# Kernel tuning notes

Hardware: AMD Instinct MI355X
Metric: run time of the kernel (lower is better)

## Reference

```python
import jax, jax.numpy as jnp
import numpy as np

D_MODEL = 1024
EXPERT_SIZE = 512
N_EXPERTS = 8
GROUP_SIZE = 32
BATCH = 32
SEQ = 2048
TEMPERATURE = 1.0


def setup_inputs() -> dict:
    key = jax.random.key(0)
    k_x, k_l1, k_l2, k_c = jax.random.split(key, 4)
    x = jax.random.normal(k_x, (BATCH, SEQ, D_MODEL), dtype=jnp.float32)
    # truncated-normal-style init approximated with normal scaled by 1/sqrt(fan_in)
    lin1 = jax.random.normal(k_l1, (N_EXPERTS, D_MODEL, EXPERT_SIZE), dtype=jnp.float32) * (D_MODEL ** -0.5)
    lin2 = jax.random.normal(k_l2, (N_EXPERTS, EXPERT_SIZE, D_MODEL), dtype=jnp.float32) * (EXPERT_SIZE ** -0.5)
    controller = jax.random.normal(k_c, (D_MODEL, N_EXPERTS), dtype=jnp.float32) * (D_MODEL ** -0.5)
    return {"x": x, "lin1": lin1, "lin2": lin2, "controller": controller}


def reference(x, lin1, lin2, controller):
    B, S, D = x.shape
    # group_tokens: sparsity_dim=0 -> transpose to (S, B, D), split batch into groups
    xg = jnp.transpose(x, (1, 0, 2)).reshape(S, B // GROUP_SIZE, GROUP_SIZE, D)  # (s, g, k, d)
    # controller logits, softmax over the group (token) axis k (dim=-2)
    logits = jnp.einsum("sgkd,de->sgke", xg, controller) / TEMPERATURE
    merge_w = jax.nn.softmax(logits, axis=-2)  # (s, g, k, e)
    emit_w = merge_w  # default: emit softmax over tokens, same temp -> reuse
    # merge: weighted sum of tokens per expert
    merged = jnp.einsum("sgke,sgkd->sged", merge_w, xg)  # (s, g, e, d)
    # per-expert MLP
    h = jax.nn.relu(jnp.einsum("sged,edf->sgef", merged, lin1))  # (s, g, e, f)
    expert_out = jnp.einsum("sgef,efd->sged", h, lin2)  # (s, g, e, d)
    # emit back to tokens
    out = jnp.einsum("sgke,sged->sgkd", emit_w, expert_out)  # (s, g, k, d)
    # redistribute: (S, B, D) -> (B, S, D)
    return jnp.transpose(out.reshape(S, B, D), (1, 0, 2))
```

## Files before the change

### kernel.cpp

```cpp
#include <hip/hip_runtime.h>
#include <hip/hip_bf16.h>

#define SS 2048
#define BB 32
#define DD 1024
#define FF 512
#define EE 8

typedef __attribute__((ext_vector_type(8))) short short8;
typedef __attribute__((ext_vector_type(8))) unsigned short ushort8v;
typedef __attribute__((ext_vector_type(4))) unsigned short ushort4v;
typedef __attribute__((ext_vector_type(4))) float f32x4;

__device__ inline unsigned short f2bf(float f) {
  union { float f; unsigned u; } v; v.f = f;
  return (unsigned short)((v.u + 0x7FFFu + ((v.u >> 16) & 1u)) >> 16);
}
__device__ inline float bf2f(unsigned short h) {
  union { unsigned u; float f; } v; v.u = ((unsigned)h) << 16;
  return v.f;
}

__global__ __launch_bounds__(256) void ctrl_transpose(
    const float* __restrict__ ctrl, float* __restrict__ ctrlT) {
  int i = blockIdx.x * 256 + threadIdx.x;
  int e = i >> 10, d = i & 1023;
  ctrlT[i] = ctrl[(size_t)d * EE + e];
}

__global__ __launch_bounds__(256) void transpose_bf16(
    const float* __restrict__ in, unsigned short* __restrict__ out, int K, int N) {
  __shared__ float tile[32][33];
  int e = blockIdx.z;
  const float* inp = in + (size_t)e * K * N;
  unsigned short* outp = out + (size_t)e * K * N;
  int k0 = blockIdx.x * 32, n0 = blockIdx.y * 32;
  int tx = threadIdx.x;
  int ty = threadIdx.y;
#pragma unroll
  for (int i = 0; i < 4; i++) {
    int k = ty + i * 8;
    tile[k][tx] = inp[(size_t)(k0 + k) * N + n0 + tx];
  }
  __syncthreads();
#pragma unroll
  for (int i = 0; i < 4; i++) {
    int n = ty + i * 8;
    outp[(size_t)(n0 + n) * K + k0 + tx] = f2bf(tile[tx][n]);
  }
}

__global__ __launch_bounds__(512) void ctrl_logits(
    const float* __restrict__ x,
    const float* __restrict__ ctrlT,
    float* __restrict__ lg) {
  int s = blockIdx.x;
  int t = threadIdx.x, lane = t & 63, w = t >> 6;
  __shared__ __align__(16) float cs[EE * DD];
  for (int i = t; i < EE * DD / 4; i += 512)
    *(float4*)&cs[i * 4] = *(const float4*)&ctrlT[i * 4];
  __syncthreads();

  float acc[4][8] = {};
#pragma unroll
  for (int i = 0; i < 4; i++) {
    int dbase = lane * 4 + i * 256;
    float4 c4[8];
#pragma unroll
    for (int e = 0; e < 8; e++) c4[e] = *(const float4*)&cs[e * DD + dbase];
#pragma unroll
    for (int j = 0; j < 4; j++) {
      int k = w * 4 + j;
      float4 xv = *(const float4*)&x[((size_t)k * SS + s) * DD + dbase];
#pragma unroll
      for (int e = 0; e < 8; e++)
        acc[j][e] += xv.x * c4[e].x + xv.y * c4[e].y + xv.z * c4[e].z + xv.w * c4[e].w;
    }
  }
#pragma unroll
  for (int off = 1; off < 64; off <<= 1)
#pragma unroll
    for (int j = 0; j < 4; j++)
#pragma unroll
      for (int e = 0; e < 8; e++)
        acc[j][e] += __shfl_xor(acc[j][e], off, 64);
  if (lane == 0) {
#pragma unroll
    for (int j = 0; j < 4; j++) {
      int k = w * 4 + j;
      float4 lo = {acc[j][0], acc[j][1], acc[j][2], acc[j][3]};
      float4 hi = {acc[j][4], acc[j][5], acc[j][6], acc[j][7]};
      float* p = &lg[((size_t)s * BB + k) * EE];
      *(float4*)p = lo;
      *(float4*)(p + 4) = hi;
    }
  }
}

__global__ __launch_bounds__(256) void softmax_merge(
    const float* __restrict__ x,
    const float* __restrict__ lg,
    unsigned short* __restrict__ merged,
    float* __restrict__ mw) {
  int s = blockIdx.x;
  int t = threadIdx.x;
  __shared__ __align__(16) float wl[BB][EE];
  wl[t >> 3][t & 7] = lg[(size_t)s * BB * EE + t];
  __syncthreads();
  if (t < 32) {
    float lgv[8], mx[8], p[8], sm[8];
#pragma unroll
    for (int e = 0; e < 8; e++) { lgv[e] = wl[t][e]; mx[e] = lgv[e]; }
#pragma unroll
    for (int off = 1; off < 32; off <<= 1)
#pragma unroll
      for (int e = 0; e < 8; e++)
        mx[e] = fmaxf(mx[e], __shfl_xor(mx[e], off, 64));
#pragma unroll
    for (int e = 0; e < 8; e++) { p[e] = __expf(lgv[e] - mx[e]); sm[e] = p[e]; }
#pragma unroll
    for (int off = 1; off < 32; off <<= 1)
#pragma unroll
      for (int e = 0; e < 8; e++)
        sm[e] += __shfl_xor(sm[e], off, 64);
    float wv[8];
#pragma unroll
    for (int e = 0; e < 8; e++) { wv[e] = p[e] / sm[e]; wl[t][e] = wv[e]; }
    float4 mv0 = {wv[0], wv[1], wv[2], wv[3]};
    float4 mv1 = {wv[4], wv[5], wv[6], wv[7]};
    float* mwp = &mw[((size_t)s * BB + t) * EE];
    *(float4*)mwp = mv0;
    *(float4*)(mwp + 4) = mv1;
  }
  __syncthreads();

  int d0 = t * 4;
  float a[8][4] = {};
#pragma unroll 4
  for (int k = 0; k < 32; k++) {
    float4 xv = *(const float4*)&x[((size_t)k * SS + s) * DD + d0];
    float4 wA = *(const float4*)&wl[k][0];
    float4 wB = *(const float4*)&wl[k][4];
    a[0][0] += wA.x * xv.x; a[0][1] += wA.x * xv.y; a[0][2] += wA.x * xv.z; a[0][3] += wA.x * xv.w;
    a[1][0] += wA.y * xv.x; a[1][1] += wA.y * xv.y; a[1][2] += wA.y * xv.z; a[1][3] += wA.y * xv.w;
    a[2][0] += wA.z * xv.x; a[2][1] += wA.z * xv.y; a[2][2] += wA.z * xv.z; a[2][3] += wA.z * xv.w;
    a[3][0] += wA.w * xv.x; a[3][1] += wA.w * xv.y; a[3][2] += wA.w * xv.z; a[3][3] += wA.w * xv.w;
    a[4][0] += wB.x * xv.x; a[4][1] += wB.x * xv.y; a[4][2] += wB.x * xv.z; a[4][3] += wB.x * xv.w;
    a[5][0] += wB.y * xv.x; a[5][1] += wB.y * xv.y; a[5][2] += wB.y * xv.z; a[5][3] += wB.y * xv.w;
    a[6][0] += wB.z * xv.x; a[6][1] += wB.z * xv.y; a[6][2] += wB.z * xv.z; a[6][3] += wB.z * xv.w;
    a[7][0] += wB.w * xv.x; a[7][1] += wB.w * xv.y; a[7][2] += wB.w * xv.z; a[7][3] += wB.w * xv.w;
  }
#pragma unroll
  for (int e = 0; e < 8; e++) {
    ushort4v pv;
    pv[0] = f2bf(a[e][0]); pv[1] = f2bf(a[e][1]);
    pv[2] = f2bf(a[e][2]); pv[3] = f2bf(a[e][3]);
    *(ushort4v*)&merged[((size_t)s * EE + e) * DD + d0] = pv;
  }
}

template <int RELU>
__global__ __launch_bounds__(256) void gemm_bt(
    const unsigned short* __restrict__ A, const unsigned short* __restrict__ Bt,
    unsigned short* __restrict__ C, int K, int N) {
  int e = blockIdx.z;
  int m0 = blockIdx.x * 128;
  int n0 = blockIdx.y * 128;
  const int lda = EE * K;
  const unsigned short* Ae = A + (size_t)e * K;
  const unsigned short* Be = Bt + (size_t)e * N * K;

  __shared__ __align__(16) unsigned short As[128 * 32];
  __shared__ __align__(16) unsigned short Bs[128 * 32];

  int t = threadIdx.x;
  int lane = t & 63, w = t >> 6;
  int wm = w >> 1, wn = w & 1;
  int lr = lane & 15;
  int kh = lane >> 4;
  int khs = kh ^ ((lr >> 1) & 3);

  f32x4 acc[4][4] = {};

  for (int kt = 0; kt < K; kt += 32) {
#pragma unroll
    for (int i = 0; i < 2; i++) {
      int c = t + i * 256;
      int r = c >> 2;
      int subg = (c & 3) ^ ((r >> 1) & 3);
      __builtin_amdgcn_global_load_lds(
          (const __attribute__((address_space(1))) void*)(Ae + (size_t)(m0 + r) * lda + kt + subg * 8),
          (__attribute__((address_space(3))) void*)(&As[c * 8]), 16, 0, 0);
      __builtin_amdgcn_global_load_lds(
          (const __attribute__((address_space(1))) void*)(Be + (size_t)(n0 + r) * K + kt + subg * 8),
          (__attribute__((address_space(3))) void*)(&Bs[c * 8]), 16, 0, 0);
    }
    __syncthreads();

    short8 af[4], bfr[4];
#pragma unroll
    for (int mi = 0; mi < 4; mi++)
      af[mi] = *(const short8*)&As[(wm * 64 + mi * 16 + lr) * 32 + khs * 8];
#pragma unroll
    for (int ni = 0; ni < 4; ni++)
      bfr[ni] = *(const short8*)&Bs[(wn * 64 + ni * 16 + lr) * 32 + khs * 8];
#pragma unroll
    for (int mi = 0; mi < 4; mi++)
#pragma unroll
      for (int ni = 0; ni < 4; ni++)
        acc[mi][ni] = __builtin_amdgcn_mfma_f32_16x16x32_bf16(af[mi], bfr[ni], acc[mi][ni], 0, 0, 0);
    __syncthreads();
  }

  int rb = (lane >> 4) * 4;
  int cb = lane & 15;
#pragma unroll
  for (int mi = 0; mi < 4; mi++)
#pragma unroll
    for (int ni = 0; ni < 4; ni++)
#pragma unroll
      for (int r = 0; r < 4; r++) {
        float v = acc[mi][ni][r];
        if (RELU) v = fmaxf(v, 0.f);
        int m = m0 + wm * 64 + mi * 16 + rb + r;
        int n = n0 + wn * 64 + ni * 16 + cb;
        C[(size_t)m * (EE * N) + (size_t)e * N + n] = f2bf(v);
      }
}

__global__ __launch_bounds__(256) void emit_out(
    const unsigned short* __restrict__ eo,
    const float* __restrict__ mw,
    float* __restrict__ out) {
  int s = blockIdx.x;
  int t = threadIdx.x;
  __shared__ float wsm[BB][EE];
  wsm[t >> 3][t & 7] = mw[(size_t)s * BB * EE + t];
  __syncthreads();
  int d0 = t * 4;
  float ev[EE][4];
#pragma unroll
  for (int e2 = 0; e2 < 8; e2++) {
    ushort4v v = *(const ushort4v*)&eo[((size_t)s * EE + e2) * DD + d0];
    ev[e2][0] = bf2f(v[0]); ev[e2][1] = bf2f(v[1]);
    ev[e2][2] = bf2f(v[2]); ev[e2][3] = bf2f(v[3]);
  }
  for (int b = 0; b < BB; b++) {
    float o0 = 0.f, o1 = 0.f, o2 = 0.f, o3 = 0.f;
#pragma unroll
    for (int e2 = 0; e2 < 8; e2++) {
      float we = wsm[b][e2];
      o0 += we * ev[e2][0]; o1 += we * ev[e2][1];
      o2 += we * ev[e2][2]; o3 += we * ev[e2][3];
    }
    float4 ov = {o0, o1, o2, o3};
    *(float4*)&out[((size_t)b * SS + s) * DD + d0] = ov;
  }
}

extern "C" void kernel_launch(void* const* d_in, const int* in_sizes, int n_in,
                              void* d_out, int out_size, void* d_ws, size_t ws_size,
                              hipStream_t stream) {
  const float* x = (const float*)d_in[0];
  const float* lin1 = (const float*)d_in[1];
  const float* lin2 = (const float*)d_in[2];
  const float* ctrl = (const float*)d_in[3];
  float* out = (float*)d_out;

  char* ws = (char*)d_ws;
  size_t off = 0;
  unsigned short* lin1t = (unsigned short*)(ws + off); off += (size_t)EE * DD * FF * 2;
  unsigned short* lin2t = (unsigned short*)(ws + off); off += (size_t)EE * FF * DD * 2;
  unsigned short* merged = (unsigned short*)(ws + off); off += (size_t)SS * EE * DD * 2;
  unsigned short* hbuf = (unsigned short*)(ws + off); off += (size_t)SS * EE * FF * 2;
  unsigned short* eo = (unsigned short*)(ws + off); off += (size_t)SS * EE * DD * 2;
  float* mw = (float*)(ws + off); off += (size_t)SS * BB * EE * 4;
  float* lg = (float*)(ws + off); off += (size_t)SS * BB * EE * 4;
  float* ctrlT = (float*)(ws + off); off += (size_t)EE * DD * 4;

  ctrl_transpose<<<32, 256, 0, stream>>>(ctrl, ctrlT);

  dim3 tb(32, 8);
  transpose_bf16<<<dim3(DD / 32, FF / 32, EE), tb, 0, stream>>>(lin1, lin1t, DD, FF);
  transpose_bf16<<<dim3(FF / 32, DD / 32, EE), tb, 0, stream>>>(lin2, lin2t, FF, DD);

  ctrl_logits<<<SS, 512, 0, stream>>>(x, ctrlT, lg);
  softmax_merge<<<SS, 256, 0, stream>>>(x, lg, merged, mw);

  gemm_bt<1><<<dim3(SS / 128, FF / 128, EE), 256, 0, stream>>>(merged, lin1t, hbuf, DD, FF);
  gemm_bt<0><<<dim3(SS / 128, DD / 128, EE), 256, 0, stream>>>(hbuf, lin2t, eo, FF, DD);

  emit_out<<<SS, 256, 0, stream>>>(eo, mw, out);
}
```

Measured before the change: 337.5 us.

## Fuse controller logits, softmax and merge into one kernel per sequence position

Merges the controller-transpose, logits, and softmax+merge kernels into a single block per sequence position. The controller transpose now happens inside each block while loading to shared memory, and the logits stay in shared memory instead of going through a global buffer. The second read of x for the merge now comes right after the first read in the same block, which may hit in cache. The merge loop is re-split over 512 threads with 2 elements each. The cost is a strided global gather of the controller in every block and fewer elements per thread.

```diff
diff --git a/kernel.cpp b/kernel.cpp
--- a/kernel.cpp
+++ b/kernel.cpp
@@ -19,13 +19,6 @@
 __device__ inline float bf2f(unsigned short h) {
   union { unsigned u; float f; } v; v.u = ((unsigned)h) << 16;
   return v.f;
-}
-
-__global__ __launch_bounds__(256) void ctrl_transpose(
-    const float* __restrict__ ctrl, float* __restrict__ ctrlT) {
-  int i = blockIdx.x * 256 + threadIdx.x;
-  int e = i >> 10, d = i & 1023;
-  ctrlT[i] = ctrl[(size_t)d * EE + e];
 }
 
 __global__ __launch_bounds__(256) void transpose_bf16(
@@ -50,15 +43,21 @@
   }
 }
 
-__global__ __launch_bounds__(512) void ctrl_logits(
+__global__ __launch_bounds__(512) void ctrl_merge_f(
     const float* __restrict__ x,
-    const float* __restrict__ ctrlT,
-    float* __restrict__ lg) {
+    const float* __restrict__ ctrl,
+    unsigned short* __restrict__ merged,
+    float* __restrict__ mw) {
   int s = blockIdx.x;
   int t = threadIdx.x, lane = t & 63, w = t >> 6;
+
   __shared__ __align__(16) float cs[EE * DD];
-  for (int i = t; i < EE * DD / 4; i += 512)
-    *(float4*)&cs[i * 4] = *(const float4*)&ctrlT[i * 4];
+  __shared__ __align__(16) float wl[BB][EE];
+
+  for (int i = t; i < DD * EE; i += 512) {
+    int d = i >> 3, e2 = i & 7;
+    cs[e2 * DD + d] = ctrl[i];
+  }
   __syncthreads();
 
   float acc[4][8] = {};
@@ -86,27 +85,13 @@
         acc[j][e] += __shfl_xor(acc[j][e], off, 64);
   if (lane == 0) {
 #pragma unroll
-    for (int j = 0; j < 4; j++) {
-      int k = w * 4 + j;
-      float4 lo = {acc[j][0], acc[j][1], acc[j][2], acc[j][3]};
-      float4 hi = {acc[j][4], acc[j][5], acc[j][6], acc[j][7]};
-      float* p = &lg[((size_t)s * BB + k) * EE];
-      *(float4*)p = lo;
-      *(float4*)(p + 4) = hi;
-    }
-  }
-}
-
-__global__ __launch_bounds__(256) void softmax_merge(
-    const float* __restrict__ x,
-    const float* __restrict__ lg,
-    unsigned short* __restrict__ merged,
-    float* __restrict__ mw) {
-  int s = blockIdx.x;
-  int t = threadIdx.x;
-  __shared__ __align__(16) float wl[BB][EE];
-  wl[t >> 3][t & 7] = lg[(size_t)s * BB * EE + t];
-  __syncthreads();
+    for (int j = 0; j < 4; j++)
+#pragma unroll
+      for (int e = 0; e < 8; e++)
+        wl[w * 4 + j][e] = acc[j][e];
+  }
+  __syncthreads();
+
   if (t < 32) {
     float lgv[8], mx[8], p[8], sm[8];
 #pragma unroll
@@ -134,28 +119,26 @@
   }
   __syncthreads();
 
-  int d0 = t * 4;
-  float a[8][4] = {};
+  int d0 = t * 2;
+  float a0[8] = {}, a1[8] = {};
 #pragma unroll 4
   for (int k = 0; k < 32; k++) {
-    float4 xv = *(const float4*)&x[((size_t)k * SS + s) * DD + d0];
+    float2 xv = *(const float2*)&x[((size_t)k * SS + s) * DD + d0];
     float4 wA = *(const float4*)&wl[k][0];
     float4 wB = *(const float4*)&wl[k][4];
-    a[0][0] += wA.x * xv.x; a[0][1] += wA.x * xv.y; a[0][2] += wA.x * xv.z; a[0][3] += wA.x * xv.w;
-    a[1][0] += wA.y * xv.x; a[1][1] += wA.y * xv.y; a[1][2] += wA.y * xv.z; a[1][3] += wA.y * xv.w;
-    a[2][0] += wA.z * xv.x; a[2][1] += wA.z * xv.y; a[2][2] += wA.z * xv.z; a[2][3] += wA.z * xv.w;
-    a[3][0] += wA.w * xv.x; a[3][1] += wA.w * xv.y; a[3][2] += wA.w * xv.z; a[3][3] += wA.w * xv.w;
-    a[4][0] += wB.x * xv.x; a[4][1] += wB.x * xv.y; a[4][2] += wB.x * xv.z; a[4][3] += wB.x * xv.w;
-    a[5][0] += wB.y * xv.x; a[5][1] += wB.y * xv.y; a[5][2] += wB.y * xv.z; a[5][3] += wB.y * xv.w;
-    a[6][0] += wB.z * xv.x; a[6][1] += wB.z * xv.y; a[6][2] += wB.z * xv.z; a[6][3] += wB.z * xv.w;
-    a[7][0] += wB.w * xv.x; a[7][1] += wB.w * xv.y; a[7][2] += wB.w * xv.z; a[7][3] += wB.w * xv.w;
+    a0[0] += wA.x * xv.x; a1[0] += wA.x * xv.y;
+    a0[1] += wA.y * xv.x; a1[1] += wA.y * xv.y;
+    a0[2] += wA.z * xv.x; a1[2] += wA.z * xv.y;
+    a0[3] += wA.w * xv.x; a1[3] += wA.w * xv.y;
+    a0[4] += wB.x * xv.x; a1[4] += wB.x * xv.y;
+    a0[5] += wB.y * xv.x; a1[5] += wB.y * xv.y;
+    a0[6] += wB.z * xv.x; a1[6] += wB.z * xv.y;
+    a0[7] += wB.w * xv.x; a1[7] += wB.w * xv.y;
   }
 #pragma unroll
   for (int e = 0; e < 8; e++) {
-    ushort4v pv;
-    pv[0] = f2bf(a[e][0]); pv[1] = f2bf(a[e][1]);
-    pv[2] = f2bf(a[e][2]); pv[3] = f2bf(a[e][3]);
-    *(ushort4v*)&merged[((size_t)s * EE + e) * DD + d0] = pv;
+    unsigned pm = (unsigned)f2bf(a0[e]) | ((unsigned)f2bf(a1[e]) << 16);
+    *(unsigned*)&merged[((size_t)s * EE + e) * DD + d0] = pm;
   }
 }
 
@@ -275,17 +258,12 @@
   unsigned short* hbuf = (unsigned short*)(ws + off); off += (size_t)SS * EE * FF * 2;
   unsigned short* eo = (unsigned short*)(ws + off); off += (size_t)SS * EE * DD * 2;
   float* mw = (float*)(ws + off); off += (size_t)SS * BB * EE * 4;
-  float* lg = (float*)(ws + off); off += (size_t)SS * BB * EE * 4;
-  float* ctrlT = (float*)(ws + off); off += (size_t)EE * DD * 4;
-
-  ctrl_transpose<<<32, 256, 0, stream>>>(ctrl, ctrlT);
 
   dim3 tb(32, 8);
   transpose_bf16<<<dim3(DD / 32, FF / 32, EE), tb, 0, stream>>>(lin1, lin1t, DD, FF);
   transpose_bf16<<<dim3(FF / 32, DD / 32, EE), tb, 0, stream>>>(lin2, lin2t, FF, DD);
 
-  ctrl_logits<<<SS, 512, 0, stream>>>(x, ctrlT, lg);
-  softmax_merge<<<SS, 256, 0, stream>>>(x, lg, merged, mw);
+  ctrl_merge_f<<<SS, 512, 0, stream>>>(x, ctrl, merged, mw);
 
   gemm_bt<1><<<dim3(SS / 128, FF / 128, EE), 256, 0, stream>>>(merged, lin1t, hbuf, DD, FF);
   gemm_bt<0><<<dim3(SS / 128, DD / 128, EE), 256, 0, stream>>>(hbuf, lin2t, eo, FF, DD);
```

After: 333.2 us. Within noise of the previous version (-1.3%).

## Restructure controller logits over contiguous token rows and split softmax from merge

Applied to the files above, without the earlier changes.

The logits kernel now has each block process 64 contiguous rows of x, with 16 lanes per row, instead of one sequence position gathering 32 strided rows. The controller is loaded straight into XOR-swizzled shared memory, which removes the separate ctrl_transpose launch. Softmax moves into its own small kernel and the merge kernel just reads the finished weights. This aims to make x reads coalesced and cut shuffle-reduction depth, at the cost of one extra launch and reloading the 32 KB controller into every one of 1024 blocks.

```diff
diff --git a/kernel.cpp b/kernel.cpp
--- a/kernel.cpp
+++ b/kernel.cpp
@@ -19,13 +19,6 @@
 __device__ inline float bf2f(unsigned short h) {
   union { unsigned u; float f; } v; v.u = ((unsigned)h) << 16;
   return v.f;
-}
-
-__global__ __launch_bounds__(256) void ctrl_transpose(
-    const float* __restrict__ ctrl, float* __restrict__ ctrlT) {
-  int i = blockIdx.x * 256 + threadIdx.x;
-  int e = i >> 10, d = i & 1023;
-  ctrlT[i] = ctrl[(size_t)d * EE + e];
 }
 
 __global__ __launch_bounds__(256) void transpose_bf16(
@@ -50,90 +43,100 @@
   }
 }
 
-__global__ __launch_bounds__(512) void ctrl_logits(
+__global__ __launch_bounds__(256) void logits_k(
     const float* __restrict__ x,
-    const float* __restrict__ ctrlT,
-    float* __restrict__ lg) {
-  int s = blockIdx.x;
-  int t = threadIdx.x, lane = t & 63, w = t >> 6;
+    const float* __restrict__ ctrl,
+    float* __restrict__ lgT) {
+  int t = threadIdx.x;
   __shared__ __align__(16) float cs[EE * DD];
-  for (int i = t; i < EE * DD / 4; i += 512)
-    *(float4*)&cs[i * 4] = *(const float4*)&ctrlT[i * 4];
-  __syncthreads();
-
+  for (int i = t; i < DD * EE; i += 256) {
+    int d = i >> 3, e = i & 7;
+    cs[e * DD + (d ^ (((d >> 6) & 7) << 2))] = ctrl[i];
+  }
+  __syncthreads();
+
+  int g = t >> 4, c = t & 15;
+  int m0 = blockIdx.x * 64 + g * 4;
+  const float* xr = x + (size_t)m0 * DD;
   float acc[4][8] = {};
-#pragma unroll
-  for (int i = 0; i < 4; i++) {
-    int dbase = lane * 4 + i * 256;
+#pragma unroll 4
+  for (int i = 0; i < 16; i++) {
+    int db = c * 4 + i * 64;
     float4 c4[8];
 #pragma unroll
-    for (int e = 0; e < 8; e++) c4[e] = *(const float4*)&cs[e * DD + dbase];
-#pragma unroll
-    for (int j = 0; j < 4; j++) {
-      int k = w * 4 + j;
-      float4 xv = *(const float4*)&x[((size_t)k * SS + s) * DD + dbase];
+    for (int e = 0; e < 8; e++)
+      c4[e] = *(const float4*)&cs[e * DD + i * 64 + ((c ^ (i & 7)) << 2)];
+#pragma unroll
+    for (int r = 0; r < 4; r++) {
+      float4 xv = *(const float4*)&xr[(size_t)r * DD + db];
 #pragma unroll
       for (int e = 0; e < 8; e++)
-        acc[j][e] += xv.x * c4[e].x + xv.y * c4[e].y + xv.z * c4[e].z + xv.w * c4[e].w;
-    }
-  }
-#pragma unroll
-  for (int off = 1; off < 64; off <<= 1)
-#pragma unroll
-    for (int j = 0; j < 4; j++)
+        acc[r][e] += xv.x * c4[e].x + xv.y * c4[e].y + xv.z * c4[e].z + xv.w * c4[e].w;
+    }
+  }
+#pragma unroll
+  for (int off = 1; off < 16; off <<= 1)
+#pragma unroll
+    for (int r = 0; r < 4; r++)
 #pragma unroll
       for (int e = 0; e < 8; e++)
-        acc[j][e] += __shfl_xor(acc[j][e], off, 64);
-  if (lane == 0) {
-#pragma unroll
-    for (int j = 0; j < 4; j++) {
-      int k = w * 4 + j;
-      float4 lo = {acc[j][0], acc[j][1], acc[j][2], acc[j][3]};
-      float4 hi = {acc[j][4], acc[j][5], acc[j][6], acc[j][7]};
-      float* p = &lg[((size_t)s * BB + k) * EE];
+        acc[r][e] += __shfl_xor(acc[r][e], off, 64);
+  if (c == 0) {
+#pragma unroll
+    for (int r = 0; r < 4; r++) {
+      int m = m0 + r;
+      int s = m & (SS - 1), k = m >> 11;
+      float* p = &lgT[((size_t)s * BB + k) * EE];
+      float4 lo = {acc[r][0], acc[r][1], acc[r][2], acc[r][3]};
+      float4 hi = {acc[r][4], acc[r][5], acc[r][6], acc[r][7]};
       *(float4*)p = lo;
       *(float4*)(p + 4) = hi;
     }
   }
 }
 
-__global__ __launch_bounds__(256) void softmax_merge(
+__global__ __launch_bounds__(256) void softmax_k(
+    const float* __restrict__ lgT,
+    float* __restrict__ mw) {
+  int t = threadIdx.x;
+  int sl = t >> 5, k = t & 31;
+  size_t s = (size_t)blockIdx.x * 8 + sl;
+  const float* p = &lgT[(s * BB + k) * EE];
+  float v[8];
+  float4 lo = *(const float4*)p, hi = *(const float4*)(p + 4);
+  v[0]=lo.x; v[1]=lo.y; v[2]=lo.z; v[3]=lo.w; v[4]=hi.x; v[5]=hi.y; v[6]=hi.z; v[7]=hi.w;
+  float mx[8];
+#pragma unroll
+  for (int e = 0; e < 8; e++) mx[e] = v[e];
+#pragma unroll
+  for (int off = 1; off < 32; off <<= 1)
+#pragma unroll
+    for (int e = 0; e < 8; e++)
+      mx[e] = fmaxf(mx[e], __shfl_xor(mx[e], off, 64));
+  float pr[8], sm[8];
+#pragma unroll
+  for (int e = 0; e < 8; e++) { pr[e] = __expf(v[e] - mx[e]); sm[e] = pr[e]; }
+#pragma unroll
+  for (int off = 1; off < 32; off <<= 1)
+#pragma unroll
+    for (int e = 0; e < 8; e++)
+      sm[e] += __shfl_xor(sm[e], off, 64);
+  float4 o0 = {pr[0]/sm[0], pr[1]/sm[1], pr[2]/sm[2], pr[3]/sm[3]};
+  float4 o1 = {pr[4]/sm[4], pr[5]/sm[5], pr[6]/sm[6], pr[7]/sm[7]};
+  float* q = &mw[(s * BB + k) * EE];
+  *(float4*)q = o0;
+  *(float4*)(q + 4) = o1;
+}
+
+__global__ __launch_bounds__(256) void merge_v(
     const float* __restrict__ x,
-    const float* __restrict__ lg,
-    unsigned short* __restrict__ merged,
-    float* __restrict__ mw) {
+    const float* __restrict__ mw,
+    unsigned short* __restrict__ merged) {
   int s = blockIdx.x;
   int t = threadIdx.x;
   __shared__ __align__(16) float wl[BB][EE];
-  wl[t >> 3][t & 7] = lg[(size_t)s * BB * EE + t];
-  __syncthreads();
-  if (t < 32) {
-    float lgv[8], mx[8], p[8], sm[8];
-#pragma unroll
-    for (int e = 0; e < 8; e++) { lgv[e] = wl[t][e]; mx[e] = lgv[e]; }
-#pragma unroll
-    for (int off = 1; off < 32; off <<= 1)
-#pragma unroll
-      for (int e = 0; e < 8; e++)
-        mx[e] = fmaxf(mx[e], __shfl_xor(mx[e], off, 64));
-#pragma unroll
-    for (int e = 0; e < 8; e++) { p[e] = __expf(lgv[e] - mx[e]); sm[e] = p[e]; }
-#pragma unroll
-    for (int off = 1; off < 32; off <<= 1)
-#pragma unroll
-      for (int e = 0; e < 8; e++)
-        sm[e] += __shfl_xor(sm[e], off, 64);
-    float wv[8];
-#pragma unroll
-    for (int e = 0; e < 8; e++) { wv[e] = p[e] / sm[e]; wl[t][e] = wv[e]; }
-    float4 mv0 = {wv[0], wv[1], wv[2], wv[3]};
-    float4 mv1 = {wv[4], wv[5], wv[6], wv[7]};
-    float* mwp = &mw[((size_t)s * BB + t) * EE];
-    *(float4*)mwp = mv0;
-    *(float4*)(mwp + 4) = mv1;
-  }
-  __syncthreads();
-
+  wl[t >> 3][t & 7] = mw[(size_t)s * BB * EE + t];
+  __syncthreads();
   int d0 = t * 4;
   float a[8][4] = {};
 #pragma unroll 4
@@ -275,17 +278,15 @@
   unsigned short* hbuf = (unsigned short*)(ws + off); off += (size_t)SS * EE * FF * 2;
   unsigned short* eo = (unsigned short*)(ws + off); off += (size_t)SS * EE * DD * 2;
   float* mw = (float*)(ws + off); off += (size_t)SS * BB * EE * 4;
-  float* lg = (float*)(ws + off); off += (size_t)SS * BB * EE * 4;
-  float* ctrlT = (float*)(ws + off); off += (size_t)EE * DD * 4;
-
-  ctrl_transpose<<<32, 256, 0, stream>>>(ctrl, ctrlT);
+  float* lgT = (float*)(ws + off); off += (size_t)SS * BB * EE * 4;
 
   dim3 tb(32, 8);
   transpose_bf16<<<dim3(DD / 32, FF / 32, EE), tb, 0, stream>>>(lin1, lin1t, DD, FF);
   transpose_bf16<<<dim3(FF / 32, DD / 32, EE), tb, 0, stream>>>(lin2, lin2t, FF, DD);
 
-  ctrl_logits<<<SS, 512, 0, stream>>>(x, ctrlT, lg);
-  softmax_merge<<<SS, 256, 0, stream>>>(x, lg, merged, mw);
+  logits_k<<<(SS * BB) / 64, 256, 0, stream>>>(x, ctrl, lgT);
+  softmax_k<<<SS / 8, 256, 0, stream>>>(lgT, mw);
+  merge_v<<<SS, 256, 0, stream>>>(x, mw, merged);
 
   gemm_bt<1><<<dim3(SS / 128, FF / 128, EE), 256, 0, stream>>>(merged, lin1t, hbuf, DD, FF);
   gemm_bt<0><<<dim3(SS / 128, DD / 128, EE), 256, 0, stream>>>(hbuf, lin2t, eo, FF, DD);
```

Measured after the change: 338.9 us. No clear change (+0.4%).
